# Kernel tuning notes

Hardware: AMD Instinct MI355X
Metric: run time of the kernel (lower is better)

## Reference

```python
import jax, jax.numpy as jnp
import numpy as np

B, V, H, K, T = 1024, 50000, 100, 200, 32768
BN_EPS = 1e-5


def _bn(x, g, b):
    # BatchNorm1d in training mode: per-feature batch statistics (biased var).
    m = x.mean(axis=0)
    v = x.var(axis=0)
    return g * (x - m) * jax.lax.rsqrt(v + BN_EPS) + b


def setup_inputs() -> dict:
    key = jax.random.key(0)
    ks = jax.random.split(key, 8)
    s = 0.02  # init scale
    return {
        'bows': jax.random.uniform(ks[0], (B, V), dtype=jnp.float32),
        'eps': jax.random.normal(ks[1], (B, K), dtype=jnp.float32),
        'ne_tokens': jax.random.randint(ks[2], (T,), 0, V, dtype=jnp.int32),
        'fc1_w': jax.random.normal(ks[3], (V, H), dtype=jnp.float32) * s,
        'fc1_b': jnp.zeros((H,), jnp.float32),
        'fc2_w': jax.random.normal(ks[4], (H, H), dtype=jnp.float32) * s,
        'fc2_b': jnp.zeros((H,), jnp.float32),
        'mu_w': jax.random.normal(ks[5], (H, K), dtype=jnp.float32) * s,
        'mu_b': jnp.zeros((K,), jnp.float32),
        'bn_mu_g': jnp.ones((K,), jnp.float32),
        'bn_mu_b': jnp.zeros((K,), jnp.float32),
        'sig_w': jax.random.normal(ks[6], (H, K), dtype=jnp.float32) * s,
        'sig_b': jnp.zeros((K,), jnp.float32),
        'bn_sig_g': jnp.ones((K,), jnp.float32),
        'bn_sig_b': jnp.zeros((K,), jnp.float32),
        'beta_w': jax.random.normal(ks[7], (K, V), dtype=jnp.float32) * s,
        'beta_b': jnp.zeros((V,), jnp.float32),
        'bn_beta_g': jnp.ones((V,), jnp.float32),
        'bn_beta_b': jnp.zeros((V,), jnp.float32),
    }


def reference(bows, eps, ne_tokens, fc1_w, fc1_b, fc2_w, fc2_b,
              mu_w, mu_b, bn_mu_g, bn_mu_b, sig_w, sig_b, bn_sig_g, bn_sig_b,
              beta_w, beta_b, bn_beta_g, bn_beta_b):
    # ProportionEncoder (dropout = identity in eval)
    h = jax.nn.softplus(bows @ fc1_w + fc1_b)            # [B,H]
    h = jax.nn.softplus(h @ fc2_w + fc2_b)               # [B,H]
    prop_mu = _bn(h @ mu_w + mu_b, bn_mu_g, bn_mu_b)     # [B,K]
    prop_sigma = jnp.exp(0.5 * _bn(h @ sig_w + sig_b, bn_sig_g, bn_sig_b))
    # LogNormal reparameterized sample: theta = exp(mu + sigma * eps)
    theta = jnp.exp(prop_mu + prop_sigma * eps)          # [B,K]
    # NeTopicDecoder: softmax(bn(linear(theta))) over vocab
    logits = _bn(theta @ beta_w + beta_b, bn_beta_g, bn_beta_b)  # [B,V]
    log_beta = jax.nn.log_softmax(logits, axis=1)        # [B,V]
    # Flattened per-NE Categorical log-prob: each obs token broadcasts over the
    # article plate, so per-article loglik = sum_t log_beta[:, ne_tokens[t]].
    loglik = jnp.take(log_beta, ne_tokens, axis=1).sum(axis=1)   # [B]
    return loglik
```

## Files before the change

### kernel.cpp

```cpp
#include <hip/hip_runtime.h>
#include <hip/hip_bf16.h>


using bf16x8 = __attribute__((ext_vector_type(8))) __bf16;
using f32x4  = __attribute__((ext_vector_type(4))) float;

#define MROWS 1024
#define VDIM  50000
#define HDIM  100
#define HP    112
#define KDIM  200
#define KP    224
#define TTOK  32768
#define KPAD1 50432
#define NCH   64
#define CHLEN 800
#define EBLK  782

__device__ __forceinline__ f32x4 mfma16(bf16x8 a, bf16x8 b, f32x4 c) {
  return __builtin_amdgcn_mfma_f32_16x16x32_bf16(a, b, c, 0, 0, 0);
}
__device__ __forceinline__ float softplus_f(float x) {
  return x > 20.f ? x : log1pf(__expf(x));
}

__global__ void k_zero(float* __restrict__ cnt) {
  int id = blockIdx.x * 256 + threadIdx.x;
  if (id < VDIM) cnt[id] = 0.f;
}
__global__ void k_hist(const int* __restrict__ tok, float* __restrict__ cnt) {
  int id = blockIdx.x * 256 + threadIdx.x;
  if (id < TTOK) atomicAdd(&cnt[tok[id]], 1.f);
}

__global__ __launch_bounds__(256) void k_fc1t(const float* __restrict__ w, __bf16* __restrict__ out) {
  __shared__ float tile[32][33];
  int kt = blockIdx.x, ct = blockIdx.y;
  int t = threadIdx.x;
  #pragma unroll
  for (int i = 0; i < 4; ++i) {
    int idx = t + i * 256;
    int lr = idx >> 5, lc = idx & 31;
    int gk = kt * 32 + lr, gc = ct * 32 + lc;
    tile[lr][lc] = (gk < VDIM && gc < HDIM) ? w[(size_t)gk * HDIM + gc] : 0.f;
  }
  __syncthreads();
  #pragma unroll
  for (int i = 0; i < 4; ++i) {
    int idx = t + i * 256;
    int lc = idx >> 5, lr = idx & 31;
    int gc = ct * 32 + lc, gk = kt * 32 + lr;
    if (gc < HP) out[(size_t)gc * KPAD1 + gk] = (__bf16)tile[lr][lc];
  }
}

__global__ __launch_bounds__(256, 4) void k_gemm1(const float* __restrict__ bows,
    const __bf16* __restrict__ fc1T, float* __restrict__ partial) {
  const int wave = threadIdx.x >> 6, lane = threadIdx.x & 63;
  const int lrow = lane & 15, lgrp = lane >> 4;
  const int rowbase = blockIdx.x * 64 + wave * 16;
  const int row = rowbase + lrow;
  const int ch = blockIdx.y;
  const int k0 = ch * CHLEN;
  const int kend = min(k0 + CHLEN, VDIM);
  const int nsteps = (kend - k0 + 31) >> 5;
  f32x4 acc[7] = {};
  const float* ap = bows + (size_t)row * VDIM;
  for (int s = 0; s < nsteps; ++s) {
    const int kl = k0 + s * 32 + lgrp * 8;
    bf16x8 a;
    if (kl + 8 <= VDIM) {
      f32x4 x0 = *(const f32x4*)(ap + kl);
      f32x4 x1 = *(const f32x4*)(ap + kl + 4);
      #pragma unroll
      for (int j = 0; j < 4; ++j) { a[j] = (__bf16)x0[j]; a[j + 4] = (__bf16)x1[j]; }
    } else {
      #pragma unroll
      for (int j = 0; j < 8; ++j) a[j] = (__bf16)((kl + j < VDIM) ? ap[kl + j] : 0.f);
    }
    #pragma unroll
    for (int n = 0; n < 7; ++n) {
      bf16x8 b = *(const bf16x8*)(fc1T + (size_t)(n * 16 + lrow) * KPAD1 + kl);
      acc[n] = mfma16(a, b, acc[n]);
    }
  }
  float* pp = partial + (size_t)ch * MROWS * HP;
  #pragma unroll
  for (int n = 0; n < 7; ++n) {
    #pragma unroll
    for (int r = 0; r < 4; ++r) {
      int rr = rowbase + lgrp * 4 + r;
      pp[(size_t)rr * HP + n * 16 + lrow] = acc[n][r];
    }
  }
}

__global__ void k_h1(const float* __restrict__ partial, const float* __restrict__ fc1_b,
                     float* __restrict__ h1) {
  int id = blockIdx.x * 256 + threadIdx.x;
  if (id >= MROWS * HDIM) return;
  int row = id / HDIM, h = id % HDIM;
  float s = fc1_b[h];
  #pragma unroll 4
  for (int c = 0; c < NCH; ++c) s += partial[((size_t)c * MROWS + row) * HP + h];
  h1[id] = softplus_f(s);
}

__global__ __launch_bounds__(256) void k_mlp(const float* __restrict__ h1,
    const float* __restrict__ fc2_w, const float* __restrict__ fc2_b,
    const float* __restrict__ mu_w, const float* __restrict__ sig_w,
    float* __restrict__ mu_lin, float* __restrict__ sig_lin) {
  __shared__ float h1r[HDIM], h2r[HDIM];
  int row = blockIdx.x, t = threadIdx.x;
  if (t < HDIM) h1r[t] = h1[(size_t)row * HDIM + t];
  __syncthreads();
  if (t < HDIM) {
    float s = fc2_b[t];
    #pragma unroll 4
    for (int k = 0; k < HDIM; ++k) s += h1r[k] * fc2_w[k * HDIM + t];
    h2r[t] = softplus_f(s);
  }
  __syncthreads();
  if (t < KDIM) {
    float sm = 0.f, ss = 0.f;
    #pragma unroll 4
    for (int k = 0; k < HDIM; ++k) {
      float h = h2r[k];
      sm += h * mu_w[k * KDIM + t];
      ss += h * sig_w[k * KDIM + t];
    }
    mu_lin[(size_t)row * KDIM + t] = sm;
    sig_lin[(size_t)row * KDIM + t] = ss;
  }
}

__global__ __launch_bounds__(256) void k_bnstats(const float* __restrict__ mu_lin,
    const float* __restrict__ sig_lin, const float* __restrict__ bn_mu_g,
    const float* __restrict__ bn_mu_b, const float* __restrict__ bn_sig_g,
    const float* __restrict__ bn_sig_b, float* __restrict__ bnsc, float* __restrict__ bnsh) {
  int bid = blockIdx.x;
  int mat = bid / KDIM, col = bid % KDIM;
  const float* src = mat ? sig_lin : mu_lin;
  int t = threadIdx.x;
  float s = 0.f, q = 0.f;
  for (int b = t; b < MROWS; b += 256) {
    float v = src[(size_t)b * KDIM + col];
    s += v; q += v * v;
  }
  #pragma unroll
  for (int d = 1; d < 64; d <<= 1) { s += __shfl_xor(s, d, 64); q += __shfl_xor(q, d, 64); }
  __shared__ float ls[4], lq[4];
  if ((t & 63) == 0) { ls[t >> 6] = s; lq[t >> 6] = q; }
  __syncthreads();
  if (t == 0) {
    s = ls[0] + ls[1] + ls[2] + ls[3];
    q = lq[0] + lq[1] + lq[2] + lq[3];
    float mean = s * (1.f / MROWS);
    float var = q * (1.f / MROWS) - mean * mean;
    float g = mat ? bn_sig_g[col] : bn_mu_g[col];
    float bb = mat ? bn_sig_b[col] : bn_mu_b[col];
    float sc = g * rsqrtf(var + 1e-5f);
    bnsc[mat * KDIM + col] = sc;
    bnsh[mat * KDIM + col] = bb - sc * mean;
  }
}

__global__ void k_theta(const float* __restrict__ mu_lin, const float* __restrict__ sig_lin,
    const float* __restrict__ eps, const float* __restrict__ bnsc, const float* __restrict__ bnsh,
    float* __restrict__ theta) {
  int id = blockIdx.x * 256 + threadIdx.x;
  if (id >= MROWS * KDIM) return;
  int k = id % KDIM;
  float mz = mu_lin[id] * bnsc[k] + bnsh[k];
  float sz = sig_lin[id] * bnsc[KDIM + k] + bnsh[KDIM + k];
  theta[id] = __expf(mz + __expf(0.5f * sz) * eps[id]);
}

__global__ __launch_bounds__(256) void k_tbar(const float* __restrict__ theta, float* __restrict__ tbar) {
  int col = blockIdx.x, t = threadIdx.x;
  float s = 0.f;
  for (int b = t; b < MROWS; b += 256) s += theta[(size_t)b * KDIM + col];
  #pragma unroll
  for (int d = 1; d < 64; d <<= 1) s += __shfl_xor(s, d, 64);
  __shared__ float ls[4];
  if ((t & 63) == 0) ls[t >> 6] = s;
  __syncthreads();
  if (t == 0) tbar[col] = (ls[0] + ls[1] + ls[2] + ls[3]) * (1.f / MROWS);
}

__global__ void k_center(const float* __restrict__ theta, const float* __restrict__ tbar,
                         __bf16* __restrict__ thetac) {
  int id = blockIdx.x * 256 + threadIdx.x;
  if (id >= MROWS * KP) return;
  int b = id / KP, kp = id % KP;
  thetac[id] = (kp < KDIM) ? (__bf16)(theta[(size_t)b * KDIM + kp] - tbar[kp]) : (__bf16)0.f;
}

__global__ __launch_bounds__(512, 2) void k_decode(
    const __bf16* __restrict__ thetac,
    const float* __restrict__ beta_w,
    const float* __restrict__ bn_g, const float* __restrict__ bn_b,
    const float* __restrict__ cnt,
    float* __restrict__ part_e, float* __restrict__ part_t) {
  __shared__ __bf16 ldsW[32][232];
  __shared__ float red[8][32];
  __shared__ float s_s[32], s_bb[32], s_ct[32];
  const int tid = threadIdx.x;
  const int wave = tid >> 6, lane = tid & 63;
  const int lrow = lane & 15, lgrp = lane >> 4;
  float esum[8] = {0, 0, 0, 0, 0, 0, 0, 0};
  float tsum[8] = {0, 0, 0, 0, 0, 0, 0, 0};
  const int cbase = blockIdx.x * 64;
  const __bf16* tp = thetac + (size_t)(wave * 128 + lrow) * KP + lgrp * 8;

  #pragma unroll 1
  for (int chunk = 0; chunk < 2; ++chunk) {
    const int cb = cbase + chunk * 32;
    if (cb >= VDIM) break;
    #pragma unroll
    for (int p = 0; p < 14; ++p) {
      int idx = p * 512 + tid;
      int k = idx >> 5, c = idx & 31;
      float v = (k < KDIM && cb + c < VDIM) ? beta_w[(size_t)k * VDIM + cb + c] : 0.f;
      ldsW[c][k] = (__bf16)v;
    }
    __syncthreads();
    f32x4 acc[2][8];
    #pragma unroll
    for (int mf = 0; mf < 2; ++mf)
      #pragma unroll
      for (int nf = 0; nf < 8; ++nf) acc[mf][nf] = (f32x4){0, 0, 0, 0};
    #pragma unroll
    for (int ks = 0; ks < 7; ++ks) {
      bf16x8 a0 = *(const bf16x8*)&ldsW[lrow][ks * 32 + lgrp * 8];
      bf16x8 a1 = *(const bf16x8*)&ldsW[16 + lrow][ks * 32 + lgrp * 8];
      #pragma unroll
      for (int nf = 0; nf < 8; ++nf) {
        bf16x8 b = *(const bf16x8*)(tp + (size_t)nf * 16 * KP + ks * 32);
        acc[0][nf] = mfma16(a0, b, acc[0][nf]);
        acc[1][nf] = mfma16(a1, b, acc[1][nf]);
      }
    }
    float vs[2][4];
    #pragma unroll
    for (int mf = 0; mf < 2; ++mf)
      #pragma unroll
      for (int r = 0; r < 4; ++r) {
        float v = 0.f;
        #pragma unroll
        for (int nf = 0; nf < 8; ++nf) { float d = acc[mf][nf][r]; v += d * d; }
        #pragma unroll
        for (int d = 1; d <= 8; d <<= 1) v += __shfl_xor(v, d, 64);
        vs[mf][r] = v;
      }
    if (lrow == 0) {
      #pragma unroll
      for (int mf = 0; mf < 2; ++mf)
        #pragma unroll
        for (int r = 0; r < 4; ++r)
          red[wave][mf * 16 + lgrp * 4 + r] = vs[mf][r];
    }
    __syncthreads();
    if (tid < 32) {
      float v = 0.f;
      #pragma unroll
      for (int w8 = 0; w8 < 8; ++w8) v += red[w8][tid];
      float var = v * (1.f / 1024.f);
      int col = cb + tid;
      bool valid = col < VDIM;
      float g = valid ? bn_g[col] : 0.f;
      float bb = valid ? bn_b[col] : -87.f;
      float ct = valid ? cnt[col] : 0.f;
      s_s[tid] = g * rsqrtf(var + 1e-5f);
      s_bb[tid] = bb;
      s_ct[tid] = ct;
    }
    __syncthreads();
    #pragma unroll
    for (int mf = 0; mf < 2; ++mf)
      #pragma unroll
      for (int r = 0; r < 4; ++r) {
        int col = mf * 16 + lgrp * 4 + r;
        float s = s_s[col], bb = s_bb[col], ct = s_ct[col];
        #pragma unroll
        for (int nf = 0; nf < 8; ++nf) {
          float z = s * acc[mf][nf][r] + bb;
          esum[nf] += __expf(z);
          tsum[nf] += ct * z;
        }
      }
    __syncthreads();
  }
  #pragma unroll
  for (int nf = 0; nf < 8; ++nf) {
    float e = esum[nf], t = tsum[nf];
    e += __shfl_xor(e, 16, 64); e += __shfl_xor(e, 32, 64);
    t += __shfl_xor(t, 16, 64); t += __shfl_xor(t, 32, 64);
    if (lgrp == 0) {
      int row = wave * 128 + nf * 16 + lrow;
      part_e[(size_t)blockIdx.x * MROWS + row] = e;
      part_t[(size_t)blockIdx.x * MROWS + row] = t;
    }
  }
}

__global__ __launch_bounds__(256) void k_final(const float* __restrict__ part_e,
    const float* __restrict__ part_t, float* __restrict__ out) {
  __shared__ float se[8][32], st[8][32];
  int t = threadIdx.x;
  int rloc = t & 31, g = t >> 5;
  int row = blockIdx.x * 32 + rloc;
  float e = 0.f, s = 0.f;
  for (int blk = g; blk < EBLK; blk += 8) {
    e += part_e[(size_t)blk * MROWS + row];
    s += part_t[(size_t)blk * MROWS + row];
  }
  se[g][rloc] = e; st[g][rloc] = s;
  __syncthreads();
  if (t < 32) {
    float et = 0.f, tt = 0.f;
    #pragma unroll
    for (int i = 0; i < 8; ++i) { et += se[i][t]; tt += st[i][t]; }
    out[blockIdx.x * 32 + t] = tt - 32768.f * logf(et);
  }
}

extern "C" void kernel_launch(void* const* d_in, const int* in_sizes, int n_in,
                              void* d_out, int out_size, void* d_ws, size_t ws_size,
                              hipStream_t stream) {
  (void)in_sizes; (void)n_in; (void)out_size; (void)ws_size;
  const float* bows      = (const float*)d_in[0];
  const float* eps       = (const float*)d_in[1];
  const int*   toks      = (const int*)d_in[2];
  const float* fc1_w     = (const float*)d_in[3];
  const float* fc1_b     = (const float*)d_in[4];
  const float* fc2_w     = (const float*)d_in[5];
  const float* fc2_b     = (const float*)d_in[6];
  const float* mu_w      = (const float*)d_in[7];
  const float* bn_mu_g   = (const float*)d_in[9];
  const float* bn_mu_b   = (const float*)d_in[10];
  const float* sig_w     = (const float*)d_in[11];
  const float* bn_sig_g  = (const float*)d_in[13];
  const float* bn_sig_b  = (const float*)d_in[14];
  const float* beta_w    = (const float*)d_in[15];
  const float* bn_beta_g = (const float*)d_in[17];
  const float* bn_beta_b = (const float*)d_in[18];

  char* w = (char*)d_ws;
  auto alloc = [&](size_t b) { char* p = w; w += (b + 255) & ~(size_t)255; return p; };
  __bf16* fc1T   = (__bf16*)alloc((size_t)HP * KPAD1 * 2);
  float* partial = (float*)alloc((size_t)NCH * MROWS * HP * 4);
  float* h1      = (float*)alloc((size_t)MROWS * HDIM * 4);
  float* mu_lin  = (float*)alloc((size_t)MROWS * KDIM * 4);
  float* sig_lin = (float*)alloc((size_t)MROWS * KDIM * 4);
  float* bnsc    = (float*)alloc(2 * KDIM * 4);
  float* bnsh    = (float*)alloc(2 * KDIM * 4);
  float* theta   = (float*)alloc((size_t)MROWS * KDIM * 4);
  float* tbar    = (float*)alloc(KDIM * 4);
  __bf16* thetac = (__bf16*)alloc((size_t)MROWS * KP * 2);
  float* cnt     = (float*)alloc((size_t)VDIM * 4);
  float* part_e  = (float*)alloc((size_t)EBLK * MROWS * 4);
  float* part_t  = (float*)alloc((size_t)EBLK * MROWS * 4);

  k_zero<<<(VDIM + 255) / 256, 256, 0, stream>>>(cnt);
  k_hist<<<(TTOK + 255) / 256, 256, 0, stream>>>(toks, cnt);
  k_fc1t<<<dim3(KPAD1 / 32, 4), 256, 0, stream>>>(fc1_w, fc1T);
  k_gemm1<<<dim3(16, NCH), 256, 0, stream>>>(bows, fc1T, partial);
  k_h1<<<(MROWS * HDIM + 255) / 256, 256, 0, stream>>>(partial, fc1_b, h1);
  k_mlp<<<MROWS, 256, 0, stream>>>(h1, fc2_w, fc2_b, mu_w, sig_w, mu_lin, sig_lin);
  k_bnstats<<<2 * KDIM, 256, 0, stream>>>(mu_lin, sig_lin, bn_mu_g, bn_mu_b, bn_sig_g, bn_sig_b, bnsc, bnsh);
  k_theta<<<(MROWS * KDIM + 255) / 256, 256, 0, stream>>>(mu_lin, sig_lin, eps, bnsc, bnsh, theta);
  k_tbar<<<KDIM, 256, 0, stream>>>(theta, tbar);
  k_center<<<(MROWS * KP + 255) / 256, 256, 0, stream>>>(theta, tbar, thetac);
  k_decode<<<EBLK, 512, 0, stream>>>(thetac, beta_w, bn_beta_g, bn_beta_b, cnt, part_e, part_t);
  k_final<<<MROWS / 32, 256, 0, stream>>>(part_e, part_t, (float*)d_out);
}
```

Measured before the change: 731.4 us.

## Pre-transpose beta_w to bf16 [V,K] and feed decode MFMA from global directly

Adds a transpose kernel that converts beta_w into a padded bf16 [V,KP] layout, so the decoder loads its weight fragments straight from global memory instead of doing strided fp32 loads, transposing through LDS, and converting per block. The decode loop is restructured into four 16-column chunks per block with a single accumulator set, dropping the LDS weight tile and one barrier per chunk. In exchange it adds an extra launch and a roughly 22 MB write and read of the transposed weights, and the MFMA work per chunk halves while the number of chunks doubles.

New measurement: 709.3 us. 1.03x faster.

```diff
diff --git a/kernel.cpp b/kernel.cpp
--- a/kernel.cpp
+++ b/kernel.cpp
@@ -7,6 +7,7 @@
 
 #define MROWS 1024
 #define VDIM  50000
+#define VPAD  50048
 #define HDIM  100
 #define HP    112
 #define KDIM  200
@@ -15,6 +16,7 @@
 #define KPAD1 50432
 #define NCH   64
 #define CHLEN 800
+#define CPB   64
 #define EBLK  782
 
 __device__ __forceinline__ f32x4 mfma16(bf16x8 a, bf16x8 b, f32x4 c) {
@@ -51,6 +53,27 @@
     int lc = idx >> 5, lr = idx & 31;
     int gc = ct * 32 + lc, gk = kt * 32 + lr;
     if (gc < HP) out[(size_t)gc * KPAD1 + gk] = (__bf16)tile[lr][lc];
+  }
+}
+
+__global__ __launch_bounds__(256) void k_wt(const float* __restrict__ w, __bf16* __restrict__ out) {
+  __shared__ float tile[32][33];
+  int vt = blockIdx.x, kt = blockIdx.y;
+  int t = threadIdx.x;
+  #pragma unroll
+  for (int i = 0; i < 4; ++i) {
+    int idx = t + i * 256;
+    int lr = idx >> 5, lc = idx & 31;
+    int gk = kt * 32 + lr, gv = vt * 32 + lc;
+    tile[lr][lc] = (gk < KDIM && gv < VDIM) ? w[(size_t)gk * VDIM + gv] : 0.f;
+  }
+  __syncthreads();
+  #pragma unroll
+  for (int i = 0; i < 4; ++i) {
+    int idx = t + i * 256;
+    int lk = idx & 31, lv = idx >> 5;
+    int gv = vt * 32 + lv, gk = kt * 32 + lk;
+    if (gv < VPAD) out[(size_t)gv * KP + gk] = (__bf16)tile[lk][lv];
   }
 }
 
@@ -198,70 +221,46 @@
 
 __global__ __launch_bounds__(512, 2) void k_decode(
     const __bf16* __restrict__ thetac,
-    const float* __restrict__ beta_w,
+    const __bf16* __restrict__ Wt,
     const float* __restrict__ bn_g, const float* __restrict__ bn_b,
     const float* __restrict__ cnt,
     float* __restrict__ part_e, float* __restrict__ part_t) {
-  __shared__ __bf16 ldsW[32][232];
-  __shared__ float red[8][32];
-  __shared__ float s_s[32], s_bb[32], s_ct[32];
+  __shared__ float red[8][16];
+  __shared__ float s_s[16], s_bb[16], s_ct[16];
   const int tid = threadIdx.x;
   const int wave = tid >> 6, lane = tid & 63;
   const int lrow = lane & 15, lgrp = lane >> 4;
   float esum[8] = {0, 0, 0, 0, 0, 0, 0, 0};
   float tsum[8] = {0, 0, 0, 0, 0, 0, 0, 0};
-  const int cbase = blockIdx.x * 64;
   const __bf16* tp = thetac + (size_t)(wave * 128 + lrow) * KP + lgrp * 8;
 
   #pragma unroll 1
-  for (int chunk = 0; chunk < 2; ++chunk) {
-    const int cb = cbase + chunk * 32;
-    if (cb >= VDIM) break;
-    #pragma unroll
-    for (int p = 0; p < 14; ++p) {
-      int idx = p * 512 + tid;
-      int k = idx >> 5, c = idx & 31;
-      float v = (k < KDIM && cb + c < VDIM) ? beta_w[(size_t)k * VDIM + cb + c] : 0.f;
-      ldsW[c][k] = (__bf16)v;
-    }
-    __syncthreads();
-    f32x4 acc[2][8];
-    #pragma unroll
-    for (int mf = 0; mf < 2; ++mf)
-      #pragma unroll
-      for (int nf = 0; nf < 8; ++nf) acc[mf][nf] = (f32x4){0, 0, 0, 0};
+  for (int chunk = 0; chunk < 4; ++chunk) {
+    const int cb = blockIdx.x * CPB + chunk * 16;
+    const __bf16* wp = Wt + (size_t)(cb + lrow) * KP + lgrp * 8;
+    f32x4 acc[8];
+    #pragma unroll
+    for (int nf = 0; nf < 8; ++nf) acc[nf] = (f32x4){0, 0, 0, 0};
     #pragma unroll
     for (int ks = 0; ks < 7; ++ks) {
-      bf16x8 a0 = *(const bf16x8*)&ldsW[lrow][ks * 32 + lgrp * 8];
-      bf16x8 a1 = *(const bf16x8*)&ldsW[16 + lrow][ks * 32 + lgrp * 8];
+      bf16x8 a = *(const bf16x8*)(wp + ks * 32);
       #pragma unroll
       for (int nf = 0; nf < 8; ++nf) {
         bf16x8 b = *(const bf16x8*)(tp + (size_t)nf * 16 * KP + ks * 32);
-        acc[0][nf] = mfma16(a0, b, acc[0][nf]);
-        acc[1][nf] = mfma16(a1, b, acc[1][nf]);
+        acc[nf] = mfma16(a, b, acc[nf]);
       }
     }
-    float vs[2][4];
-    #pragma unroll
-    for (int mf = 0; mf < 2; ++mf)
-      #pragma unroll
-      for (int r = 0; r < 4; ++r) {
-        float v = 0.f;
-        #pragma unroll
-        for (int nf = 0; nf < 8; ++nf) { float d = acc[mf][nf][r]; v += d * d; }
-        #pragma unroll
-        for (int d = 1; d <= 8; d <<= 1) v += __shfl_xor(v, d, 64);
-        vs[mf][r] = v;
-      }
-    if (lrow == 0) {
-      #pragma unroll
-      for (int mf = 0; mf < 2; ++mf)
-        #pragma unroll
-        for (int r = 0; r < 4; ++r)
-          red[wave][mf * 16 + lgrp * 4 + r] = vs[mf][r];
+    #pragma unroll
+    for (int r = 0; r < 4; ++r) {
+      float v = 0.f;
+      #pragma unroll
+      for (int nf = 0; nf < 8; ++nf) { float d = acc[nf][r]; v += d * d; }
+      #pragma unroll
+      for (int d = 1; d <= 8; d <<= 1) v += __shfl_xor(v, d, 64);
+      if (lrow == 0) red[wave][lgrp * 4 + r] = v;
     }
     __syncthreads();
-    if (tid < 32) {
+    if (tid < 16) {
       float v = 0.f;
       #pragma unroll
       for (int w8 = 0; w8 < 8; ++w8) v += red[w8][tid];
@@ -277,19 +276,16 @@
     }
     __syncthreads();
     #pragma unroll
-    for (int mf = 0; mf < 2; ++mf)
-      #pragma unroll
-      for (int r = 0; r < 4; ++r) {
-        int col = mf * 16 + lgrp * 4 + r;
-        float s = s_s[col], bb = s_bb[col], ct = s_ct[col];
-        #pragma unroll
-        for (int nf = 0; nf < 8; ++nf) {
-          float z = s * acc[mf][nf][r] + bb;
-          esum[nf] += __expf(z);
-          tsum[nf] += ct * z;
-        }
+    for (int r = 0; r < 4; ++r) {
+      int col = lgrp * 4 + r;
+      float s = s_s[col], bb = s_bb[col], ct = s_ct[col];
+      #pragma unroll
+      for (int nf = 0; nf < 8; ++nf) {
+        float z = s * acc[nf][r] + bb;
+        esum[nf] += __expf(z);
+        tsum[nf] += ct * z;
       }
-    __syncthreads();
+    }
   }
   #pragma unroll
   for (int nf = 0; nf < 8; ++nf) {
@@ -349,6 +345,7 @@
   char* w = (char*)d_ws;
   auto alloc = [&](size_t b) { char* p = w; w += (b + 255) & ~(size_t)255; return p; };
   __bf16* fc1T   = (__bf16*)alloc((size_t)HP * KPAD1 * 2);
+  __bf16* Wt     = (__bf16*)alloc((size_t)VPAD * KP * 2);
   float* partial = (float*)alloc((size_t)NCH * MROWS * HP * 4);
   float* h1      = (float*)alloc((size_t)MROWS * HDIM * 4);
   float* mu_lin  = (float*)alloc((size_t)MROWS * KDIM * 4);
@@ -365,6 +362,7 @@
   k_zero<<<(VDIM + 255) / 256, 256, 0, stream>>>(cnt);
   k_hist<<<(TTOK + 255) / 256, 256, 0, stream>>>(toks, cnt);
   k_fc1t<<<dim3(KPAD1 / 32, 4), 256, 0, stream>>>(fc1_w, fc1T);
+  k_wt<<<dim3(VPAD / 32, KP / 32), 256, 0, stream>>>(beta_w, Wt);
   k_gemm1<<<dim3(16, NCH), 256, 0, stream>>>(bows, fc1T, partial);
   k_h1<<<(MROWS * HDIM + 255) / 256, 256, 0, stream>>>(partial, fc1_b, h1);
   k_mlp<<<MROWS, 256, 0, stream>>>(h1, fc2_w, fc2_b, mu_w, sig_w, mu_lin, sig_lin);
@@ -372,6 +370,6 @@
   k_theta<<<(MROWS * KDIM + 255) / 256, 256, 0, stream>>>(mu_lin, sig_lin, eps, bnsc, bnsh, theta);
   k_tbar<<<KDIM, 256, 0, stream>>>(theta, tbar);
   k_center<<<(MROWS * KP + 255) / 256, 256, 0, stream>>>(theta, tbar, thetac);
-  k_decode<<<EBLK, 512, 0, stream>>>(thetac, beta_w, bn_beta_g, bn_beta_b, cnt, part_e, part_t);
+  k_decode<<<EBLK, 512, 0, stream>>>(thetac, Wt, bn_beta_g, bn_beta_b, cnt, part_e, part_t);
   k_final<<<MROWS / 32, 256, 0, stream>>>(part_e, part_t, (float*)d_out);
 }
```
